# Optimization experiments

Hardware: AMD Instinct MI355X
Metric: run time of the kernel (lower is better)

Reference implementation:

```python
import jax, jax.numpy as jnp
import numpy as np

MAX_LENGTH = 10
SOS = 0


def setup_inputs() -> dict:
    key = jax.random.key(0)
    ks = jax.random.split(key, 16)
    B, S, H, V = 64, 128, 1024, 32000
    sc = 0.02
    return {
        "encoder_outputs": jax.random.normal(ks[0], (B, S, H), jnp.float32),
        "encoder_hidden": jax.random.normal(ks[1], (1, B, H), jnp.float32),
        "target_tensor": jax.random.randint(ks[2], (B, MAX_LENGTH), 0, V),
        "embedding": jax.random.normal(ks[3], (V, H), jnp.float32) * sc,
        "Wa_w": jax.random.normal(ks[4], (H, H), jnp.float32) * sc,
        "Wa_b": jnp.zeros((H,), jnp.float32),
        "Ua_w": jax.random.normal(ks[5], (H, H), jnp.float32) * sc,
        "Ua_b": jnp.zeros((H,), jnp.float32),
        "Va_w": jax.random.normal(ks[6], (1, H), jnp.float32) * sc,
        "Va_b": jnp.zeros((1,), jnp.float32),
        "gru_wi": jax.random.normal(ks[7], (3 * H, 2 * H), jnp.float32) * sc,
        "gru_wh": jax.random.normal(ks[8], (3 * H, H), jnp.float32) * sc,
        "gru_bi": jnp.zeros((3 * H,), jnp.float32),
        "gru_bh": jnp.zeros((3 * H,), jnp.float32),
        "out_w": jax.random.normal(ks[9], (V, H), jnp.float32) * sc,
        "out_b": jnp.zeros((V,), jnp.float32),
    }


def reference(encoder_outputs, encoder_hidden, target_tensor, embedding,
              Wa_w, Wa_b, Ua_w, Ua_b, Va_w, Va_b,
              gru_wi, gru_wh, gru_bi, gru_bh, out_w, out_b):
    B, S, H = encoder_outputs.shape
    # teacher-forced input tokens: [SOS, tgt_0, ..., tgt_{T-2}]
    tokens = jnp.concatenate(
        [jnp.full((B, 1), SOS, dtype=target_tensor.dtype),
         target_tensor[:, :MAX_LENGTH - 1]], axis=1)  # [B, T]
    emb_seq = embedding[tokens]                         # [B, T, H] (dropout = identity)
    # precompute Ua(keys), shared across steps
    Ua_keys = jnp.einsum('bsh,kh->bsk', encoder_outputs, Ua_w) + Ua_b  # [B,S,H]
    va = Va_w[0]

    def step(h, emb_t):  # h: [B,H], emb_t: [B,H]
        q = h @ Wa_w.T + Wa_b                                   # [B,H]
        scores = jnp.einsum('bsh,h->bs', jnp.tanh(q[:, None, :] + Ua_keys), va) + Va_b[0]
        w = jax.nn.softmax(scores, axis=-1)                     # [B,S]
        ctx = jnp.einsum('bs,bsh->bh', w, encoder_outputs)      # [B,H]
        x = jnp.concatenate([emb_t, ctx], axis=-1)              # [B,2H]
        gi = x @ gru_wi.T + gru_bi                              # [B,3H]
        gh = h @ gru_wh.T + gru_bh
        r = jax.nn.sigmoid(gi[:, :H] + gh[:, :H])
        z = jax.nn.sigmoid(gi[:, H:2 * H] + gh[:, H:2 * H])
        n = jnp.tanh(gi[:, 2 * H:] + r * gh[:, 2 * H:])
        h_new = (1.0 - z) * n + z * h
        return h_new, (h_new, w)

    h0 = encoder_hidden[0]  # [B,H]
    h_final, (outs, attns) = jax.lax.scan(step, h0, jnp.swapaxes(emb_seq, 0, 1))
    outs = jnp.swapaxes(outs, 0, 1)                 # [B,T,H]
    attns = jnp.swapaxes(attns, 0, 1)               # [B,T,S]
    logits = jnp.einsum('bth,vh->btv', outs, out_w) + out_b
    log_probs = jax.nn.log_softmax(logits, axis=-1)  # [B,T,V]
    return log_probs, h_final[None], attns
```

## Files before the change

kernel.cpp:

```cpp
#include <hip/hip_runtime.h>
#include <hip/hip_bf16.h>
#include <cstddef>

#define B 64
#define S 128
#define H 1024
#define V 32000
#define T 10
#define H3 3072
#define NCHUNK 250

typedef __bf16 bf16x8 __attribute__((ext_vector_type(8)));
typedef float f32x4 __attribute__((ext_vector_type(4)));
typedef unsigned short ushort8v __attribute__((ext_vector_type(8)));

__device__ inline unsigned short f2b(float f) {
    __hip_bfloat16 h = __float2bfloat16(f);
    return *reinterpret_cast<unsigned short*>(&h);
}
__device__ inline float b2f(unsigned short u) {
    return __uint_as_float(((unsigned)u) << 16);
}
__device__ inline float fast_tanh(float x) {
    float e = __expf(2.f * x);
    return 1.f - 2.f * __builtin_amdgcn_rcpf(e + 1.f);
}
__device__ inline float fast_sigmoid(float x) {
    return __builtin_amdgcn_rcpf(1.f + __expf(-x));
}

__device__ inline int xcd_swz(int orig, int nwg) {
    int q = nwg >> 3, r = nwg & 7;
    int xcd = orig & 7, idx = orig >> 3;
    int base = (xcd < r) ? xcd * (q + 1) : r * (q + 1) + (xcd - r) * q;
    return base + idx;
}

#define PREP_NB 52240
__global__ void prep_kernel(const float* __restrict__ enc, unsigned short* __restrict__ enc_bf,
                            const float* __restrict__ out_w, unsigned short* __restrict__ outw_bf,
                            const float* __restrict__ Ua_w, unsigned short* __restrict__ Ua_bf,
                            const float* __restrict__ gwh, const float* __restrict__ Wa_w,
                            unsigned short* __restrict__ Wcat,
                            const float* __restrict__ gwi,
                            unsigned short* __restrict__ Wemb, unsigned short* __restrict__ Wctx,
                            const float* __restrict__ gbh, const float* __restrict__ Wa_b,
                            float* __restrict__ catbias,
                            const float* __restrict__ emb, const int* __restrict__ tgt,
                            unsigned short* __restrict__ embg,
                            const float* __restrict__ h0, unsigned short* __restrict__ hbf,
                            float* __restrict__ hbuf) {
    const int bid = blockIdx.x, tid = threadIdx.x;
    if (bid < 8192) {
        int i = bid * 256 + tid;
        float4 v = reinterpret_cast<const float4*>(enc)[i];
        ushort4 o = { f2b(v.x), f2b(v.y), f2b(v.z), f2b(v.w) };
        reinterpret_cast<ushort4*>(enc_bf)[i] = o;
    } else if (bid < 40192) {
        int i = (bid - 8192) * 256 + tid;
        float4 v = reinterpret_cast<const float4*>(out_w)[i];
        ushort4 o = { f2b(v.x), f2b(v.y), f2b(v.z), f2b(v.w) };
        reinterpret_cast<ushort4*>(outw_bf)[i] = o;
    } else if (bid < 41216) {
        int i = (bid - 40192) * 256 + tid;
        float4 v = reinterpret_cast<const float4*>(Ua_w)[i];
        ushort4 o = { f2b(v.x), f2b(v.y), f2b(v.z), f2b(v.w) };
        reinterpret_cast<ushort4*>(Ua_bf)[i] = o;
    } else if (bid < 45312) {
        int i = (bid - 41216) * 256 + tid;
        int e = i * 4, n = e >> 10, k = e & 1023;
        const float* src = (n < H3) ? (gwh + (size_t)n * H + k) : (Wa_w + (size_t)(n - H3) * H + k);
        float4 v = *reinterpret_cast<const float4*>(src);
        ushort4 o = { f2b(v.x), f2b(v.y), f2b(v.z), f2b(v.w) };
        reinterpret_cast<ushort4*>(Wcat)[i] = o;
    } else if (bid < 48384) {
        int i = (bid - 45312) * 256 + tid;
        int e = i * 4, n = e >> 10, k = e & 1023;
        float4 v = *reinterpret_cast<const float4*>(gwi + (size_t)n * 2 * H + k);
        ushort4 o = { f2b(v.x), f2b(v.y), f2b(v.z), f2b(v.w) };
        reinterpret_cast<ushort4*>(Wemb)[i] = o;
    } else if (bid < 51456) {
        int i = (bid - 48384) * 256 + tid;
        int e = i * 4, n = e >> 10, k = e & 1023;
        float4 v = *reinterpret_cast<const float4*>(gwi + (size_t)n * 2 * H + H + k);
        ushort4 o = { f2b(v.x), f2b(v.y), f2b(v.z), f2b(v.w) };
        reinterpret_cast<ushort4*>(Wctx)[i] = o;
    } else if (bid < 51472) {
        int n = (bid - 51456) * 256 + tid;
        catbias[n] = (n < H3) ? gbh[n] : Wa_b[n - H3];
    } else if (bid < 52112) {
        int i = (bid - 51472) * 256 + tid;
        int e = i * 4;
        int t = e >> 16, rem = e & 65535;
        int b = rem >> 10, j = rem & 1023;
        int tok = (t == 0) ? 0 : tgt[b * T + (t - 1)];
        float4 v = *reinterpret_cast<const float4*>(emb + (size_t)tok * H + j);
        ushort4 o = { f2b(v.x), f2b(v.y), f2b(v.z), f2b(v.w) };
        *reinterpret_cast<ushort4*>(embg + ((size_t)t * B + b) * H + j) = o;
    } else if (bid < 52176) {
        int i = (bid - 52112) * 256 + tid;
        float4 v = reinterpret_cast<const float4*>(h0)[i];
        ushort4 o = { f2b(v.x), f2b(v.y), f2b(v.z), f2b(v.w) };
        reinterpret_cast<ushort4*>(hbf)[i] = o;
    } else {
        int i = (bid - 52176) * 256 + tid;
        reinterpret_cast<float4*>(hbuf)[i] = reinterpret_cast<const float4*>(h0)[i];
    }
}

struct GemmDesc {
    const unsigned short* A;
    const unsigned short* Bw;
    const float* bias;
    void* C;
    int M, N, out_bf16;
};

__global__ __launch_bounds__(512) void gemm3_kernel(GemmDesc d0, GemmDesc d1, GemmDesc d2) {
    __shared__ unsigned short As[128][72];
    __shared__ unsigned short Bs[128][72];
    const int bid = blockIdx.x;
    GemmDesc d; int local, nwg;
    if (bid < 512)       { d = d0; local = bid;        nwg = 512;  }
    else if (bid < 2048) { d = d1; local = bid - 512;  nwg = 1536; }
    else                 { d = d2; local = bid - 2048; nwg = 120;  }
    local = xcd_swz(local, nwg);
    const int mtiles = d.M >> 7;
    const int bm = (local % mtiles) << 7, bn = (local / mtiles) << 7;
    const int tid = threadIdx.x, lane = tid & 63, w = tid >> 6;
    const int wm = w >> 2, wn = w & 3;
    const int quad = lane >> 4, fr = lane & 15;
    f32x4 acc[4][2] = {};

    const int srow = tid >> 2, sc16 = (tid & 3) * 16;
    for (int k0 = 0; k0 < H; k0 += 64) {
        const unsigned short* ap = d.A + (size_t)(bm + srow) * H + k0 + sc16;
        *reinterpret_cast<bf16x8*>(&As[srow][sc16])     = *reinterpret_cast<const bf16x8*>(ap);
        *reinterpret_cast<bf16x8*>(&As[srow][sc16 + 8]) = *reinterpret_cast<const bf16x8*>(ap + 8);
        const unsigned short* bp = d.Bw + (size_t)(bn + srow) * H + k0 + sc16;
        *reinterpret_cast<bf16x8*>(&Bs[srow][sc16])     = *reinterpret_cast<const bf16x8*>(bp);
        *reinterpret_cast<bf16x8*>(&Bs[srow][sc16 + 8]) = *reinterpret_cast<const bf16x8*>(bp + 8);
        __syncthreads();
        #pragma unroll
        for (int ks = 0; ks < 2; ++ks) {
            const int kg = quad * 8 + 32 * ks;
            bf16x8 a[4], bb[2];
            #pragma unroll
            for (int m = 0; m < 4; ++m)
                a[m] = *reinterpret_cast<const bf16x8*>(&As[64 * wm + 16 * m + fr][kg]);
            #pragma unroll
            for (int n = 0; n < 2; ++n)
                bb[n] = *reinterpret_cast<const bf16x8*>(&Bs[32 * wn + 16 * n + fr][kg]);
            #pragma unroll
            for (int m = 0; m < 4; ++m)
                #pragma unroll
                for (int n = 0; n < 2; ++n)
                    acc[m][n] = __builtin_amdgcn_mfma_f32_16x16x32_bf16(a[m], bb[n], acc[m][n], 0, 0, 0);
        }
        __syncthreads();
    }
    #pragma unroll
    for (int n = 0; n < 2; ++n) {
        int col = bn + 32 * wn + 16 * n + fr;
        float bv = d.bias ? d.bias[col] : 0.f;
        #pragma unroll
        for (int m = 0; m < 4; ++m)
            #pragma unroll
            for (int i = 0; i < 4; ++i) {
                int row = bm + 64 * wm + 16 * m + quad * 4 + i;
                float v = acc[m][n][i] + bv;
                if (d.out_bf16)
                    ((unsigned short*)d.C)[(size_t)row * d.N + col] = f2b(v);
                else
                    ((float*)d.C)[(size_t)row * d.N + col] = v;
            }
    }
}

__global__ __launch_bounds__(512) void gemm_logits(const unsigned short* __restrict__ A,
                                                   const unsigned short* __restrict__ Bw,
                                                   const float* __restrict__ bias,
                                                   float* __restrict__ Cout,
                                                   float2* __restrict__ stats,
                                                   int M, int N, int K) {
    __shared__ unsigned short As[128][72];
    __shared__ unsigned short Bs[128][72];
    __shared__ float mred[128][4];
    __shared__ float sred[128][4];
    const int wg = xcd_swz(blockIdx.x, gridDim.x);
    const int mtiles = M >> 7;
    const int bm = (wg % mtiles) << 7, bn = (wg / mtiles) << 7;
    const int tid = threadIdx.x, lane = tid & 63, w = tid >> 6;
    const int wm = w >> 2, wn = w & 3;
    const int quad = lane >> 4, fr = lane & 15;
    f32x4 acc[4][2] = {};

    const int srow = tid >> 2, sc16 = (tid & 3) * 16;
    for (int k0 = 0; k0 < K; k0 += 64) {
        const unsigned short* ap = A + (size_t)(bm + srow) * K + k0 + sc16;
        *reinterpret_cast<bf16x8*>(&As[srow][sc16])     = *reinterpret_cast<const bf16x8*>(ap);
        *reinterpret_cast<bf16x8*>(&As[srow][sc16 + 8]) = *reinterpret_cast<const bf16x8*>(ap + 8);
        const unsigned short* bp = Bw + (size_t)(bn + srow) * K + k0 + sc16;
        *reinterpret_cast<bf16x8*>(&Bs[srow][sc16])     = *reinterpret_cast<const bf16x8*>(bp);
        *reinterpret_cast<bf16x8*>(&Bs[srow][sc16 + 8]) = *reinterpret_cast<const bf16x8*>(bp + 8);
        __syncthreads();
        #pragma unroll
        for (int ks = 0; ks < 2; ++ks) {
            const int kg = quad * 8 + 32 * ks;
            bf16x8 a[4], bb[2];
            #pragma unroll
            for (int m = 0; m < 4; ++m)
                a[m] = *reinterpret_cast<const bf16x8*>(&As[64 * wm + 16 * m + fr][kg]);
            #pragma unroll
            for (int n = 0; n < 2; ++n)
                bb[n] = *reinterpret_cast<const bf16x8*>(&Bs[32 * wn + 16 * n + fr][kg]);
            #pragma unroll
            for (int m = 0; m < 4; ++m)
                #pragma unroll
                for (int n = 0; n < 2; ++n)
                    acc[m][n] = __builtin_amdgcn_mfma_f32_16x16x32_bf16(a[m], bb[n], acc[m][n], 0, 0, 0);
        }
        __syncthreads();
    }

    #pragma unroll
    for (int n = 0; n < 2; ++n) {
        int col = bn + 32 * wn + 16 * n + fr;
        float bv = bias[col];
        #pragma unroll
        for (int m = 0; m < 4; ++m)
            #pragma unroll
            for (int i = 0; i < 4; ++i) {
                int row = bm + 64 * wm + 16 * m + quad * 4 + i;
                float v = acc[m][n][i] + bv;
                Cout[(size_t)row * N + col] = v;
                acc[m][n][i] = v;
            }
    }

    const int nchunk = N >> 7;
    #pragma unroll
    for (int m = 0; m < 4; ++m)
        #pragma unroll
        for (int i = 0; i < 4; ++i) {
            float x = fmaxf(acc[m][0][i], acc[m][1][i]);
            x = fmaxf(x, __shfl_xor(x, 1)); x = fmaxf(x, __shfl_xor(x, 2));
            x = fmaxf(x, __shfl_xor(x, 4)); x = fmaxf(x, __shfl_xor(x, 8));
            if (fr == 0) mred[64 * wm + 16 * m + quad * 4 + i][wn] = x;
        }
    __syncthreads();
    #pragma unroll
    for (int m = 0; m < 4; ++m)
        #pragma unroll
        for (int i = 0; i < 4; ++i) {
            int rl = 64 * wm + 16 * m + quad * 4 + i;
            float Mr = fmaxf(fmaxf(mred[rl][0], mred[rl][1]), fmaxf(mred[rl][2], mred[rl][3]));
            float sv = expf(acc[m][0][i] - Mr) + expf(acc[m][1][i] - Mr);
            sv += __shfl_xor(sv, 1); sv += __shfl_xor(sv, 2);
            sv += __shfl_xor(sv, 4); sv += __shfl_xor(sv, 8);
            if (fr == 0) sred[rl][wn] = sv;
        }
    __syncthreads();
    if (tid < 128) {
        float Mr = fmaxf(fmaxf(mred[tid][0], mred[tid][1]), fmaxf(mred[tid][2], mred[tid][3]));
        float Sv = sred[tid][0] + sred[tid][1] + sred[tid][2] + sred[tid][3];
        stats[(size_t)(bm + tid) * nchunk + (bn >> 7)] = make_float2(Mr, Sv);
    }
}

__global__ __launch_bounds__(256) void gemm_smallA(const unsigned short* __restrict__ A,
                                                   const unsigned short* __restrict__ Bw,
                                                   const float* __restrict__ bias,
                                                   float* __restrict__ Cout) {
    __shared__ unsigned short As[64][136];
    __shared__ unsigned short Bs[32][136];
    const int bn = blockIdx.x * 32;
    const int tid = threadIdx.x, lane = tid & 63, w = tid >> 6;
    const int quad = lane >> 4, fr = lane & 15;
    f32x4 acc[2] = {};

    const int srA = tid >> 2, scA = (tid & 3) * 32;
    const int srB = tid >> 3, scB = (tid & 7) * 16;
    for (int k0 = 0; k0 < H; k0 += 128) {
        const unsigned short* ap = A + (size_t)srA * H + k0 + scA;
        #pragma unroll
        for (int u = 0; u < 4; ++u)
            *reinterpret_cast<bf16x8*>(&As[srA][scA + 8 * u]) =
                *reinterpret_cast<const bf16x8*>(ap + 8 * u);
        const unsigned short* bp = Bw + (size_t)(bn + srB) * H + k0 + scB;
        *reinterpret_cast<bf16x8*>(&Bs[srB][scB])     = *reinterpret_cast<const bf16x8*>(bp);
        *reinterpret_cast<bf16x8*>(&Bs[srB][scB + 8]) = *reinterpret_cast<const bf16x8*>(bp + 8);
        __syncthreads();
        #pragma unroll
        for (int ks = 0; ks < 4; ++ks) {
            const int kg = quad * 8 + 32 * ks;
            bf16x8 a = *reinterpret_cast<const bf16x8*>(&As[16 * w + fr][kg]);
            #pragma unroll
            for (int n = 0; n < 2; ++n) {
                bf16x8 bb = *reinterpret_cast<const bf16x8*>(&Bs[16 * n + fr][kg]);
                acc[n] = __builtin_amdgcn_mfma_f32_16x16x32_bf16(a, bb, acc[n], 0, 0, 0);
            }
        }
        __syncthreads();
    }
    #pragma unroll
    for (int n = 0; n < 2; ++n) {
        int col = bn + 16 * n + fr;
        float bv = bias[col];
        #pragma unroll
        for (int i = 0; i < 4; ++i) {
            int row = 16 * w + quad * 4 + i;
            Cout[(size_t)row * 4096 + col] = acc[n][i] + bv;
        }
    }
}

__global__ __launch_bounds__(256) void stepB(const float* __restrict__ ghq,
                                             const unsigned short* __restrict__ keys,
                                             const unsigned short* __restrict__ KV,
                                             const float* __restrict__ va,
                                             const float* __restrict__ va_b,
                                             const float* __restrict__ gi_emb,
                                             float* __restrict__ h,
                                             unsigned short* __restrict__ hbf,
                                             unsigned short* __restrict__ outs_bf,
                                             float* __restrict__ attns,
                                             float* __restrict__ h_final, int t) {
    const int q = blockIdx.x, b = blockIdx.y;
    const int tid = threadIdx.x, lane = tid & 63, wv = tid >> 6;
    __shared__ float ssc[128];
    __shared__ float sw[128];
    __shared__ float red[4][64][13];

    float qv[16], vv[16];
    {
        const float* qp = ghq + (size_t)b * 4096 + H3 + lane * 16;
        const float* vp = va + lane * 16;
        #pragma unroll
        for (int j = 0; j < 16; ++j) { qv[j] = qp[j]; vv[j] = vp[j]; }
    }
    const float vab = va_b[0];
    const unsigned short* kb = keys + (size_t)b * S * H;
    for (int i = 0; i < 32; i += 2) {
        int s0 = wv * 32 + i;
        const unsigned short* kr0 = kb + (size_t)s0 * H + lane * 16;
        const unsigned short* kr1 = kr0 + H;
        ushort8v k00 = *reinterpret_cast<const ushort8v*>(kr0);
        ushort8v k01 = *reinterpret_cast<const ushort8v*>(kr0 + 8);
        ushort8v k10 = *reinterpret_cast<const ushort8v*>(kr1);
        ushort8v k11 = *reinterpret_cast<const ushort8v*>(kr1 + 8);
        float a0 = 0.f, a1 = 0.f;
        #pragma unroll
        for (int e = 0; e < 8; ++e) {
            a0 += fast_tanh(qv[e] + b2f(k00[e])) * vv[e];
            a1 += fast_tanh(qv[e] + b2f(k10[e])) * vv[e];
        }
        #pragma unroll
        for (int e = 0; e < 8; ++e) {
            a0 += fast_tanh(qv[8 + e] + b2f(k01[e])) * vv[8 + e];
            a1 += fast_tanh(qv[8 + e] + b2f(k11[e])) * vv[8 + e];
        }
        a0 += __shfl_xor(a0, 1);  a1 += __shfl_xor(a1, 1);
        a0 += __shfl_xor(a0, 2);  a1 += __shfl_xor(a1, 2);
        a0 += __shfl_xor(a0, 4);  a1 += __shfl_xor(a1, 4);
        a0 += __shfl_xor(a0, 8);  a1 += __shfl_xor(a1, 8);
        a0 += __shfl_xor(a0, 16); a1 += __shfl_xor(a1, 16);
        a0 += __shfl_xor(a0, 32); a1 += __shfl_xor(a1, 32);
        if (lane == 0) { ssc[s0] = a0 + vab; ssc[s0 + 1] = a1 + vab; }
    }
    __syncthreads();
    if (tid < 128) {
        float mx = -1e30f;
        #pragma unroll 8
        for (int s = 0; s < 128; ++s) mx = fmaxf(mx, ssc[s]);
        float sum = 0.f;
        #pragma unroll 8
        for (int s = 0; s < 128; ++s) sum += __expf(ssc[s] - mx);
        float wvv = __expf(ssc[tid] - mx) / sum;
        sw[tid] = wvv;
        if (q == 0) attns[((size_t)b * T + t) * S + tid] = wvv;
    }
    __syncthreads();

    const int j0 = q * 256 + lane * 4;
    float ar[4] = {}, az[4] = {}, an[4] = {};
    const unsigned short* kvb = KV + (size_t)b * S * H3 + j0;
    for (int i = 0; i < 32; i += 2) {
        int s0 = wv * 32 + i;
        float w0 = sw[s0], w1 = sw[s0 + 1];
        const unsigned short* r0 = kvb + (size_t)s0 * H3;
        const unsigned short* r1 = r0 + H3;
        uint2 u0a = *reinterpret_cast<const uint2*>(r0);
        uint2 u1a = *reinterpret_cast<const uint2*>(r0 + 1024);
        uint2 u2a = *reinterpret_cast<const uint2*>(r0 + 2048);
        uint2 u0b = *reinterpret_cast<const uint2*>(r1);
        uint2 u1b = *reinterpret_cast<const uint2*>(r1 + 1024);
        uint2 u2b = *reinterpret_cast<const uint2*>(r1 + 2048);
        ar[0] += w0 * b2f((unsigned short)(u0a.x & 0xffff)) + w1 * b2f((unsigned short)(u0b.x & 0xffff));
        ar[1] += w0 * b2f((unsigned short)(u0a.x >> 16))    + w1 * b2f((unsigned short)(u0b.x >> 16));
        ar[2] += w0 * b2f((unsigned short)(u0a.y & 0xffff)) + w1 * b2f((unsigned short)(u0b.y & 0xffff));
        ar[3] += w0 * b2f((unsigned short)(u0a.y >> 16))    + w1 * b2f((unsigned short)(u0b.y >> 16));
        az[0] += w0 * b2f((unsigned short)(u1a.x & 0xffff)) + w1 * b2f((unsigned short)(u1b.x & 0xffff));
        az[1] += w0 * b2f((unsigned short)(u1a.x >> 16))    + w1 * b2f((unsigned short)(u1b.x >> 16));
        az[2] += w0 * b2f((unsigned short)(u1a.y & 0xffff)) + w1 * b2f((unsigned short)(u1b.y & 0xffff));
        az[3] += w0 * b2f((unsigned short)(u1a.y >> 16))    + w1 * b2f((unsigned short)(u1b.y >> 16));
        an[0] += w0 * b2f((unsigned short)(u2a.x & 0xffff)) + w1 * b2f((unsigned short)(u2b.x & 0xffff));
        an[1] += w0 * b2f((unsigned short)(u2a.x >> 16))    + w1 * b2f((unsigned short)(u2b.x >> 16));
        an[2] += w0 * b2f((unsigned short)(u2a.y & 0xffff)) + w1 * b2f((unsigned short)(u2b.y & 0xffff));
        an[3] += w0 * b2f((unsigned short)(u2a.y >> 16))    + w1 * b2f((unsigned short)(u2b.y >> 16));
    }
    #pragma unroll
    for (int g = 0; g < 4; ++g) {
        red[wv][lane][g]     = ar[g];
        red[wv][lane][4 + g] = az[g];
        red[wv][lane][8 + g] = an[g];
    }
    __syncthreads();

    if (tid < 64) {
        float rr[4], zz[4], nn[4];
        #pragma unroll
        for (int g = 0; g < 4; ++g) {
            rr[g] = red[0][tid][g] + red[1][tid][g] + red[2][tid][g] + red[3][tid][g];
            zz[g] = red[0][tid][4+g] + red[1][tid][4+g] + red[2][tid][4+g] + red[3][tid][4+g];
            nn[g] = red[0][tid][8+g] + red[1][tid][8+g] + red[2][tid][8+g] + red[3][tid][8+g];
        }
        const int jj = q * 256 + tid * 4;
        const float* ge = gi_emb + ((size_t)t * B + b) * H3;
        const float* gh = ghq + (size_t)b * 4096;
        float geR[4], geZ[4], geN[4], ghR[4], ghZ[4], ghN[4], hv[4];
        *reinterpret_cast<float4*>(geR) = *reinterpret_cast<const float4*>(ge + jj);
        *reinterpret_cast<float4*>(geZ) = *reinterpret_cast<const float4*>(ge + 1024 + jj);
        *reinterpret_cast<float4*>(geN) = *reinterpret_cast<const float4*>(ge + 2048 + jj);
        *reinterpret_cast<float4*>(ghR) = *reinterpret_cast<const float4*>(gh + jj);
        *reinterpret_cast<float4*>(ghZ) = *reinterpret_cast<const float4*>(gh + 1024 + jj);
        *reinterpret_cast<float4*>(ghN) = *reinterpret_cast<const float4*>(gh + 2048 + jj);
        *reinterpret_cast<float4*>(hv)  = *reinterpret_cast<const float4*>(h + (size_t)b * H + jj);
        ushort4 hb;
        unsigned short* hbp = reinterpret_cast<unsigned short*>(&hb);
        #pragma unroll
        for (int i = 0; i < 4; ++i) {
            float r = fast_sigmoid(geR[i] + rr[i] + ghR[i]);
            float z = fast_sigmoid(geZ[i] + zz[i] + ghZ[i]);
            float n = fast_tanh(geN[i] + nn[i] + r * ghN[i]);
            hv[i] = (1.f - z) * n + z * hv[i];
            hbp[i] = f2b(hv[i]);
        }
        *reinterpret_cast<float4*>(h + (size_t)b * H + jj) = *reinterpret_cast<float4*>(hv);
        *reinterpret_cast<ushort4*>(hbf + (size_t)b * H + jj) = hb;
        *reinterpret_cast<ushort4*>(outs_bf + ((size_t)b * T + t) * H + jj) = hb;
        if (t == T - 1)
            *reinterpret_cast<float4*>(h_final + (size_t)b * H + jj) = *reinterpret_cast<float4*>(hv);
    }
}

__global__ void lsesub_kernel(const float2* __restrict__ stats, float* __restrict__ x) {
    const int row = blockIdx.x;
    const int tid = threadIdx.x;
    __shared__ float shm[256];
    __shared__ float shs[256];
    float mv = -1e30f, sv = 0.f;
    float2 st = make_float2(-1e30f, 0.f);
    if (tid < NCHUNK) { st = stats[(size_t)row * NCHUNK + tid]; mv = st.x; }
    shm[tid] = mv; __syncthreads();
    for (int off = 128; off > 0; off >>= 1) {
        if (tid < off) shm[tid] = fmaxf(shm[tid], shm[tid + off]);
        __syncthreads();
    }
    float M = shm[0]; __syncthreads();
    if (tid < NCHUNK) sv = st.y * expf(st.x - M);
    shs[tid] = sv; __syncthreads();
    for (int off = 128; off > 0; off >>= 1) {
        if (tid < off) shs[tid] += shs[tid + off];
        __syncthreads();
    }
    float L = M + logf(shs[0]);
    __syncthreads();
    float4* p = reinterpret_cast<float4*>(x + (size_t)row * V);
    for (int i = tid; i < V / 4; i += 256) {
        float4 v = p[i];
        v.x -= L; v.y -= L; v.z -= L; v.w -= L;
        p[i] = v;
    }
}


extern "C" void kernel_launch(void* const* d_in, const int* in_sizes, int n_in,
                              void* d_out, int out_size, void* d_ws, size_t ws_size,
                              hipStream_t stream) {
    const float* enc   = (const float*)d_in[0];
    const float* h0    = (const float*)d_in[1];
    const int*   tgt   = (const int*)d_in[2];
    const float* emb   = (const float*)d_in[3];
    const float* Wa_w  = (const float*)d_in[4];
    const float* Wa_b  = (const float*)d_in[5];
    const float* Ua_w  = (const float*)d_in[6];
    const float* Ua_b  = (const float*)d_in[7];
    const float* Va_w  = (const float*)d_in[8];
    const float* Va_b  = (const float*)d_in[9];
    const float* gwi   = (const float*)d_in[10];
    const float* gwh   = (const float*)d_in[11];
    const float* gbi   = (const float*)d_in[12];
    const float* gbh   = (const float*)d_in[13];
    const float* out_w = (const float*)d_in[14];
    const float* out_b = (const float*)d_in[15];

    float* out       = (float*)d_out;
    float* log_probs = out;
    float* h_final   = out + (size_t)B * T * V;
    float* attns     = h_final + (size_t)B * H;

    char* pp = (char*)d_ws;
    auto alloc = [&](size_t bytes) { char* r = pp; pp += (bytes + 255) & ~(size_t)255; return r; };
    unsigned short* ua_bf   = (unsigned short*)alloc((size_t)B * S * H * 2);
    unsigned short* enc_bf  = (unsigned short*)alloc((size_t)B * S * H * 2);
    unsigned short* outw_bf = (unsigned short*)alloc((size_t)V * H * 2);
    unsigned short* KV      = (unsigned short*)alloc((size_t)B * S * H3 * 2);
    unsigned short* Ua_bf   = (unsigned short*)alloc((size_t)H * H * 2);
    unsigned short* Wcat    = (unsigned short*)alloc((size_t)4096 * H * 2);
    unsigned short* Wctx    = (unsigned short*)alloc((size_t)H3 * H * 2);
    unsigned short* Wemb    = (unsigned short*)alloc((size_t)H3 * H * 2);
    float*          catbias = (float*)alloc(4096 * 4);
    unsigned short* embg    = (unsigned short*)alloc((size_t)T * B * H * 2);
    float*          gi_emb  = (float*)alloc((size_t)T * B * H3 * 4);
    float*          hbuf    = (float*)alloc((size_t)B * H * 4);
    unsigned short* hbf     = (unsigned short*)alloc((size_t)B * H * 2);
    float*          ghq     = (float*)alloc((size_t)B * 4096 * 4);
    unsigned short* outs_bf = (unsigned short*)alloc((size_t)B * T * H * 2);
    float2*         stats   = (float2*)alloc((size_t)B * T * NCHUNK * 8);

    prep_kernel<<<PREP_NB, 256, 0, stream>>>(enc, enc_bf, out_w, outw_bf, Ua_w, Ua_bf,
                                             gwh, Wa_w, Wcat, gwi, Wemb, Wctx,
                                             gbh, Wa_b, catbias, emb, tgt, embg,
                                             h0, hbf, hbuf);

    GemmDesc d0 = { enc_bf, Ua_bf, Ua_b, (void*)ua_bf,  B * S, H,  1 };
    GemmDesc d1 = { enc_bf, Wctx,  nullptr, (void*)KV,  B * S, H3, 1 };
    GemmDesc d2 = { embg,   Wemb,  gbi, (void*)gi_emb,  T * B, H3, 0 };
    gemm3_kernel<<<2168, 512, 0, stream>>>(d0, d1, d2);

    for (int t = 0; t < T; ++t) {
        gemm_smallA<<<128, 256, 0, stream>>>(hbf, Wcat, catbias, ghq);
        stepB<<<dim3(4, B), 256, 0, stream>>>(ghq, ua_bf, KV, Va_w, Va_b, gi_emb,
                                              hbuf, hbf, outs_bf, attns, h_final, t);
    }

    gemm_logits<<<(B * T / 128) * (V / 128), 512, 0, stream>>>(
        outs_bf, outw_bf, out_b, log_probs, stats, B * T, V, H);
    lsesub_kernel<<<B * T, 256, 0, stream>>>(stats, log_probs);
}
```

Baseline: 711.6 us.

## Fuse per-step GEMM and attention/GRU via grid barrier; overlap out_w conversion with GEMMs

The two per-timestep kernels (a small h×[Wgh;Wa] GEMM and the attention+GRU update) are merged into a single 256-block kernel. The blocks synchronize through an atomic-counter grid barrier, with a separate counter per step, and exchange ghq through system-scope atomic loads and stores. This halves the launches in the recurrent loop and removes the inter-kernel gaps. Separately, the bf16 conversion of out_w moves out of the prep kernel into extra blocks of the batched GEMM launch, so it can overlap with GEMM work. The spin barrier relies on all 256 blocks being co-resident, and the scalarized atomic loads may be slower than vector loads.

```diff
diff --git a/kernel.cpp b/kernel.cpp
--- a/kernel.cpp
+++ b/kernel.cpp
@@ -9,6 +9,7 @@
 #define T 10
 #define H3 3072
 #define NCHUNK 250
+#define SK_NB 256
 
 typedef __bf16 bf16x8 __attribute__((ext_vector_type(8)));
 typedef float f32x4 __attribute__((ext_vector_type(4)));
@@ -27,6 +28,18 @@
 }
 __device__ inline float fast_sigmoid(float x) {
     return __builtin_amdgcn_rcpf(1.f + __expf(-x));
+}
+__device__ inline float2 sysload_f2(const float* p) {
+    unsigned long long v = __hip_atomic_load((const unsigned long long*)p,
+                                             __ATOMIC_RELAXED, __HIP_MEMORY_SCOPE_SYSTEM);
+    float2 r;
+    r.x = __uint_as_float((unsigned)v);
+    r.y = __uint_as_float((unsigned)(v >> 32));
+    return r;
+}
+__device__ inline void sysstore_f(float* p, float v) {
+    __hip_atomic_store((unsigned*)p, __float_as_uint(v),
+                       __ATOMIC_RELAXED, __HIP_MEMORY_SCOPE_SYSTEM);
 }
 
 __device__ inline int xcd_swz(int orig, int nwg) {
@@ -36,9 +49,8 @@
     return base + idx;
 }
 
-#define PREP_NB 52240
+#define PREP_NB 20240
 __global__ void prep_kernel(const float* __restrict__ enc, unsigned short* __restrict__ enc_bf,
-                            const float* __restrict__ out_w, unsigned short* __restrict__ outw_bf,
                             const float* __restrict__ Ua_w, unsigned short* __restrict__ Ua_bf,
                             const float* __restrict__ gwh, const float* __restrict__ Wa_w,
                             unsigned short* __restrict__ Wcat,
@@ -56,40 +68,35 @@
         float4 v = reinterpret_cast<const float4*>(enc)[i];
         ushort4 o = { f2b(v.x), f2b(v.y), f2b(v.z), f2b(v.w) };
         reinterpret_cast<ushort4*>(enc_bf)[i] = o;
-    } else if (bid < 40192) {
+    } else if (bid < 9216) {
         int i = (bid - 8192) * 256 + tid;
-        float4 v = reinterpret_cast<const float4*>(out_w)[i];
-        ushort4 o = { f2b(v.x), f2b(v.y), f2b(v.z), f2b(v.w) };
-        reinterpret_cast<ushort4*>(outw_bf)[i] = o;
-    } else if (bid < 41216) {
-        int i = (bid - 40192) * 256 + tid;
         float4 v = reinterpret_cast<const float4*>(Ua_w)[i];
         ushort4 o = { f2b(v.x), f2b(v.y), f2b(v.z), f2b(v.w) };
         reinterpret_cast<ushort4*>(Ua_bf)[i] = o;
-    } else if (bid < 45312) {
-        int i = (bid - 41216) * 256 + tid;
+    } else if (bid < 13312) {
+        int i = (bid - 9216) * 256 + tid;
         int e = i * 4, n = e >> 10, k = e & 1023;
         const float* src = (n < H3) ? (gwh + (size_t)n * H + k) : (Wa_w + (size_t)(n - H3) * H + k);
         float4 v = *reinterpret_cast<const float4*>(src);
         ushort4 o = { f2b(v.x), f2b(v.y), f2b(v.z), f2b(v.w) };
         reinterpret_cast<ushort4*>(Wcat)[i] = o;
-    } else if (bid < 48384) {
-        int i = (bid - 45312) * 256 + tid;
+    } else if (bid < 16384) {
+        int i = (bid - 13312) * 256 + tid;
         int e = i * 4, n = e >> 10, k = e & 1023;
         float4 v = *reinterpret_cast<const float4*>(gwi + (size_t)n * 2 * H + k);
         ushort4 o = { f2b(v.x), f2b(v.y), f2b(v.z), f2b(v.w) };
         reinterpret_cast<ushort4*>(Wemb)[i] = o;
-    } else if (bid < 51456) {
-        int i = (bid - 48384) * 256 + tid;
+    } else if (bid < 19456) {
+        int i = (bid - 16384) * 256 + tid;
         int e = i * 4, n = e >> 10, k = e & 1023;
         float4 v = *reinterpret_cast<const float4*>(gwi + (size_t)n * 2 * H + H + k);
         ushort4 o = { f2b(v.x), f2b(v.y), f2b(v.z), f2b(v.w) };
         reinterpret_cast<ushort4*>(Wctx)[i] = o;
-    } else if (bid < 51472) {
-        int n = (bid - 51456) * 256 + tid;
+    } else if (bid < 19472) {
+        int n = (bid - 19456) * 256 + tid;
         catbias[n] = (n < H3) ? gbh[n] : Wa_b[n - H3];
-    } else if (bid < 52112) {
-        int i = (bid - 51472) * 256 + tid;
+    } else if (bid < 20112) {
+        int i = (bid - 19472) * 256 + tid;
         int e = i * 4;
         int t = e >> 16, rem = e & 65535;
         int b = rem >> 10, j = rem & 1023;
@@ -97,13 +104,13 @@
         float4 v = *reinterpret_cast<const float4*>(emb + (size_t)tok * H + j);
         ushort4 o = { f2b(v.x), f2b(v.y), f2b(v.z), f2b(v.w) };
         *reinterpret_cast<ushort4*>(embg + ((size_t)t * B + b) * H + j) = o;
-    } else if (bid < 52176) {
-        int i = (bid - 52112) * 256 + tid;
+    } else if (bid < 20176) {
+        int i = (bid - 20112) * 256 + tid;
         float4 v = reinterpret_cast<const float4*>(h0)[i];
         ushort4 o = { f2b(v.x), f2b(v.y), f2b(v.z), f2b(v.w) };
         reinterpret_cast<ushort4*>(hbf)[i] = o;
     } else {
-        int i = (bid - 52176) * 256 + tid;
+        int i = (bid - 20176) * 256 + tid;
         reinterpret_cast<float4*>(hbuf)[i] = reinterpret_cast<const float4*>(h0)[i];
     }
 }
@@ -116,10 +123,20 @@
     int M, N, out_bf16;
 };
 
-__global__ __launch_bounds__(512) void gemm3_kernel(GemmDesc d0, GemmDesc d1, GemmDesc d2) {
+__global__ __launch_bounds__(512) void gemm3_kernel(GemmDesc d0, GemmDesc d1, GemmDesc d2,
+                                                    const float* __restrict__ out_w,
+                                                    unsigned short* __restrict__ outw_bf) {
     __shared__ unsigned short As[128][72];
     __shared__ unsigned short Bs[128][72];
     const int bid = blockIdx.x;
+    const int tid = threadIdx.x;
+    if (bid >= 2168) {
+        int i = (bid - 2168) * 512 + tid;
+        float4 v = reinterpret_cast<const float4*>(out_w)[i];
+        ushort4 o = { f2b(v.x), f2b(v.y), f2b(v.z), f2b(v.w) };
+        reinterpret_cast<ushort4*>(outw_bf)[i] = o;
+        return;
+    }
     GemmDesc d; int local, nwg;
     if (bid < 512)       { d = d0; local = bid;        nwg = 512;  }
     else if (bid < 2048) { d = d1; local = bid - 512;  nwg = 1536; }
@@ -127,7 +144,7 @@
     local = xcd_swz(local, nwg);
     const int mtiles = d.M >> 7;
     const int bm = (local % mtiles) << 7, bn = (local / mtiles) << 7;
-    const int tid = threadIdx.x, lane = tid & 63, w = tid >> 6;
+    const int lane = tid & 63, w = tid >> 6;
     const int wm = w >> 2, wn = w & 3;
     const int quad = lane >> 4, fr = lane & 15;
     f32x4 acc[4][2] = {};
@@ -268,76 +285,83 @@
     }
 }
 
-__global__ __launch_bounds__(256) void gemm_smallA(const unsigned short* __restrict__ A,
-                                                   const unsigned short* __restrict__ Bw,
-                                                   const float* __restrict__ bias,
-                                                   float* __restrict__ Cout) {
+__global__ __launch_bounds__(256) void step_kernel(const unsigned short* __restrict__ hbf_in,
+                                                   const unsigned short* __restrict__ Wcat,
+                                                   const float* __restrict__ catbias,
+                                                   float* __restrict__ ghq,
+                                                   const unsigned short* __restrict__ keys,
+                                                   const unsigned short* __restrict__ KV,
+                                                   const float* __restrict__ va,
+                                                   const float* __restrict__ va_b,
+                                                   const float* __restrict__ gi_emb,
+                                                   float* __restrict__ h,
+                                                   unsigned short* __restrict__ hbf_out,
+                                                   unsigned short* __restrict__ outs_bf,
+                                                   float* __restrict__ attns,
+                                                   float* __restrict__ h_final,
+                                                   unsigned int* __restrict__ ctr, int t) {
     __shared__ unsigned short As[64][136];
-    __shared__ unsigned short Bs[32][136];
-    const int bn = blockIdx.x * 32;
-    const int tid = threadIdx.x, lane = tid & 63, w = tid >> 6;
-    const int quad = lane >> 4, fr = lane & 15;
-    f32x4 acc[2] = {};
-
-    const int srA = tid >> 2, scA = (tid & 3) * 32;
-    const int srB = tid >> 3, scB = (tid & 7) * 16;
-    for (int k0 = 0; k0 < H; k0 += 128) {
-        const unsigned short* ap = A + (size_t)srA * H + k0 + scA;
-        #pragma unroll
-        for (int u = 0; u < 4; ++u)
-            *reinterpret_cast<bf16x8*>(&As[srA][scA + 8 * u]) =
-                *reinterpret_cast<const bf16x8*>(ap + 8 * u);
-        const unsigned short* bp = Bw + (size_t)(bn + srB) * H + k0 + scB;
-        *reinterpret_cast<bf16x8*>(&Bs[srB][scB])     = *reinterpret_cast<const bf16x8*>(bp);
-        *reinterpret_cast<bf16x8*>(&Bs[srB][scB + 8]) = *reinterpret_cast<const bf16x8*>(bp + 8);
-        __syncthreads();
-        #pragma unroll
-        for (int ks = 0; ks < 4; ++ks) {
-            const int kg = quad * 8 + 32 * ks;
-            bf16x8 a = *reinterpret_cast<const bf16x8*>(&As[16 * w + fr][kg]);
-            #pragma unroll
-            for (int n = 0; n < 2; ++n) {
-                bf16x8 bb = *reinterpret_cast<const bf16x8*>(&Bs[16 * n + fr][kg]);
-                acc[n] = __builtin_amdgcn_mfma_f32_16x16x32_bf16(a, bb, acc[n], 0, 0, 0);
-            }
-        }
-        __syncthreads();
-    }
-    #pragma unroll
-    for (int n = 0; n < 2; ++n) {
-        int col = bn + 16 * n + fr;
-        float bv = bias[col];
-        #pragma unroll
-        for (int i = 0; i < 4; ++i) {
-            int row = 16 * w + quad * 4 + i;
-            Cout[(size_t)row * 4096 + col] = acc[n][i] + bv;
-        }
-    }
-}
-
-__global__ __launch_bounds__(256) void stepB(const float* __restrict__ ghq,
-                                             const unsigned short* __restrict__ keys,
-                                             const unsigned short* __restrict__ KV,
-                                             const float* __restrict__ va,
-                                             const float* __restrict__ va_b,
-                                             const float* __restrict__ gi_emb,
-                                             float* __restrict__ h,
-                                             unsigned short* __restrict__ hbf,
-                                             unsigned short* __restrict__ outs_bf,
-                                             float* __restrict__ attns,
-                                             float* __restrict__ h_final, int t) {
-    const int q = blockIdx.x, b = blockIdx.y;
-    const int tid = threadIdx.x, lane = tid & 63, wv = tid >> 6;
+    __shared__ unsigned short Bsm[16][136];
     __shared__ float ssc[128];
     __shared__ float sw[128];
     __shared__ float red[4][64][13];
-
+    const int bid = blockIdx.x;
+    const int tid = threadIdx.x, lane = tid & 63, wv = tid >> 6;
+    const int quad = lane >> 4, fr = lane & 15;
+
+    {
+        const int bn = bid * 16;
+        f32x4 acc = {};
+        const int srA = tid >> 2, scA = (tid & 3) * 32;
+        const int srB = tid >> 4, scB = (tid & 15) * 8;
+        for (int k0 = 0; k0 < H; k0 += 128) {
+            const unsigned short* ap = hbf_in + (size_t)srA * H + k0 + scA;
+            #pragma unroll
+            for (int u = 0; u < 4; ++u)
+                *reinterpret_cast<bf16x8*>(&As[srA][scA + 8 * u]) =
+                    *reinterpret_cast<const bf16x8*>(ap + 8 * u);
+            const unsigned short* bp = Wcat + (size_t)(bn + srB) * H + k0 + scB;
+            *reinterpret_cast<bf16x8*>(&Bsm[srB][scB]) = *reinterpret_cast<const bf16x8*>(bp);
+            __syncthreads();
+            #pragma unroll
+            for (int ks = 0; ks < 4; ++ks) {
+                const int kg = quad * 8 + 32 * ks;
+                bf16x8 a = *reinterpret_cast<const bf16x8*>(&As[16 * wv + fr][kg]);
+                bf16x8 bb = *reinterpret_cast<const bf16x8*>(&Bsm[fr][kg]);
+                acc = __builtin_amdgcn_mfma_f32_16x16x32_bf16(a, bb, acc, 0, 0, 0);
+            }
+            __syncthreads();
+        }
+        int col = bn + fr;
+        float bv = catbias[col];
+        #pragma unroll
+        for (int i = 0; i < 4; ++i) {
+            int row = 16 * wv + quad * 4 + i;
+            sysstore_f(&ghq[(size_t)row * 4096 + col], acc[i] + bv);
+        }
+    }
+
+    __syncthreads();
+    if (tid == 0) {
+        atomicAdd(ctr, 1u);
+        while (__hip_atomic_load(ctr, __ATOMIC_RELAXED, __HIP_MEMORY_SCOPE_AGENT) < SK_NB)
+            __builtin_amdgcn_s_sleep(1);
+    }
+    __syncthreads();
+    asm volatile("" ::: "memory");
+
+    const int q = bid & 3, b = bid >> 2;
     float qv[16], vv[16];
     {
         const float* qp = ghq + (size_t)b * 4096 + H3 + lane * 16;
         const float* vp = va + lane * 16;
         #pragma unroll
-        for (int j = 0; j < 16; ++j) { qv[j] = qp[j]; vv[j] = vp[j]; }
+        for (int j = 0; j < 8; ++j) {
+            float2 f = sysload_f2(qp + j * 2);
+            qv[j * 2] = f.x; qv[j * 2 + 1] = f.y;
+        }
+        #pragma unroll
+        for (int j = 0; j < 16; ++j) vv[j] = vp[j];
     }
     const float vab = va_b[0];
     const unsigned short* kb = keys + (size_t)b * S * H;
@@ -432,10 +456,14 @@
         *reinterpret_cast<float4*>(geR) = *reinterpret_cast<const float4*>(ge + jj);
         *reinterpret_cast<float4*>(geZ) = *reinterpret_cast<const float4*>(ge + 1024 + jj);
         *reinterpret_cast<float4*>(geN) = *reinterpret_cast<const float4*>(ge + 2048 + jj);
-        *reinterpret_cast<float4*>(ghR) = *reinterpret_cast<const float4*>(gh + jj);
-        *reinterpret_cast<float4*>(ghZ) = *reinterpret_cast<const float4*>(gh + 1024 + jj);
-        *reinterpret_cast<float4*>(ghN) = *reinterpret_cast<const float4*>(gh + 2048 + jj);
-        *reinterpret_cast<float4*>(hv)  = *reinterpret_cast<const float4*>(h + (size_t)b * H + jj);
+        float2 f;
+        f = sysload_f2(gh + jj);            ghR[0] = f.x; ghR[1] = f.y;
+        f = sysload_f2(gh + jj + 2);        ghR[2] = f.x; ghR[3] = f.y;
+        f = sysload_f2(gh + 1024 + jj);     ghZ[0] = f.x; ghZ[1] = f.y;
+        f = sysload_f2(gh + 1024 + jj + 2); ghZ[2] = f.x; ghZ[3] = f.y;
+        f = sysload_f2(gh + 2048 + jj);     ghN[0] = f.x; ghN[1] = f.y;
+        f = sysload_f2(gh + 2048 + jj + 2); ghN[2] = f.x; ghN[3] = f.y;
+        *reinterpret_cast<float4*>(hv) = *reinterpret_cast<const float4*>(h + (size_t)b * H + jj);
         ushort4 hb;
         unsigned short* hbp = reinterpret_cast<unsigned short*>(&hb);
         #pragma unroll
@@ -447,7 +475,7 @@
             hbp[i] = f2b(hv[i]);
         }
         *reinterpret_cast<float4*>(h + (size_t)b * H + jj) = *reinterpret_cast<float4*>(hv);
-        *reinterpret_cast<ushort4*>(hbf + (size_t)b * H + jj) = hb;
+        *reinterpret_cast<ushort4*>(hbf_out + (size_t)b * H + jj) = hb;
         *reinterpret_cast<ushort4*>(outs_bf + ((size_t)b * T + t) * H + jj) = hb;
         if (t == T - 1)
             *reinterpret_cast<float4*>(h_final + (size_t)b * H + jj) = *reinterpret_cast<float4*>(hv);
@@ -528,8 +556,11 @@
     float*          ghq     = (float*)alloc((size_t)B * 4096 * 4);
     unsigned short* outs_bf = (unsigned short*)alloc((size_t)B * T * H * 2);
     float2*         stats   = (float2*)alloc((size_t)B * T * NCHUNK * 8);
-
-    prep_kernel<<<PREP_NB, 256, 0, stream>>>(enc, enc_bf, out_w, outw_bf, Ua_w, Ua_bf,
+    unsigned int*   ctrs    = (unsigned int*)alloc(T * 4);
+
+    hipMemsetAsync(ctrs, 0, T * sizeof(unsigned int), stream);
+
+    prep_kernel<<<PREP_NB, 256, 0, stream>>>(enc, enc_bf, Ua_w, Ua_bf,
                                              gwh, Wa_w, Wcat, gwi, Wemb, Wctx,
                                              gbh, Wa_b, catbias, emb, tgt, embg,
                                              h0, hbf, hbuf);
@@ -537,12 +568,12 @@
     GemmDesc d0 = { enc_bf, Ua_bf, Ua_b, (void*)ua_bf,  B * S, H,  1 };
     GemmDesc d1 = { enc_bf, Wctx,  nullptr, (void*)KV,  B * S, H3, 1 };
     GemmDesc d2 = { embg,   Wemb,  gbi, (void*)gi_emb,  T * B, H3, 0 };
-    gemm3_kernel<<<2168, 512, 0, stream>>>(d0, d1, d2);
+    gemm3_kernel<<<18168, 512, 0, stream>>>(d0, d1, d2, out_w, outw_bf);
 
     for (int t = 0; t < T; ++t) {
-        gemm_smallA<<<128, 256, 0, stream>>>(hbf, Wcat, catbias, ghq);
-        stepB<<<dim3(4, B), 256, 0, stream>>>(ghq, ua_bf, KV, Va_w, Va_b, gi_emb,
-                                              hbuf, hbf, outs_bf, attns, h_final, t);
+        step_kernel<<<SK_NB, 256, 0, stream>>>(hbf, Wcat, catbias, ghq, ua_bf, KV,
+                                               Va_w, Va_b, gi_emb, hbuf, hbf, outs_bf,
+                                               attns, h_final, ctrs + t, t);
     }
 
     gemm_logits<<<(B * T / 128) * (V / 128), 512, 0, stream>>>(
```

New measurement: 734.7 us. +3.3%, slower.

## Stage GEMM tiles via direct global-to-LDS loads and overlap out_w conversion

Applied to the files above, without the earlier changes.

The bf16 GEMM kernels now load A/B tiles with global_load_lds straight into unpadded 32-wide LDS tiles, replacing register-staged 64-wide copies into padded tiles. The out_w fp32-to-bf16 conversion moves out of prep_kernel and becomes extra tail blocks of gemm3_kernel, so it can run alongside the attention-precompute GEMMs. The aim is to cut VGPR staging cost and shrink the serial prep phase. In exchange the K loop has twice as many barriers per tile, and the unpadded LDS layout may cause bank conflicts on fragment reads.

```diff
diff --git a/kernel.cpp b/kernel.cpp
--- a/kernel.cpp
+++ b/kernel.cpp
@@ -29,6 +29,12 @@
     return __builtin_amdgcn_rcpf(1.f + __expf(-x));
 }
 
+__device__ inline void gload_lds16(const void* g, void* l) {
+    __builtin_amdgcn_global_load_lds(
+        (const __attribute__((address_space(1))) void*)g,
+        (__attribute__((address_space(3))) void*)l, 16, 0, 0);
+}
+
 __device__ inline int xcd_swz(int orig, int nwg) {
     int q = nwg >> 3, r = nwg & 7;
     int xcd = orig & 7, idx = orig >> 3;
@@ -36,9 +42,8 @@
     return base + idx;
 }
 
-#define PREP_NB 52240
+#define PREP_NB 20240
 __global__ void prep_kernel(const float* __restrict__ enc, unsigned short* __restrict__ enc_bf,
-                            const float* __restrict__ out_w, unsigned short* __restrict__ outw_bf,
                             const float* __restrict__ Ua_w, unsigned short* __restrict__ Ua_bf,
                             const float* __restrict__ gwh, const float* __restrict__ Wa_w,
                             unsigned short* __restrict__ Wcat,
@@ -56,40 +61,35 @@
         float4 v = reinterpret_cast<const float4*>(enc)[i];
         ushort4 o = { f2b(v.x), f2b(v.y), f2b(v.z), f2b(v.w) };
         reinterpret_cast<ushort4*>(enc_bf)[i] = o;
-    } else if (bid < 40192) {
+    } else if (bid < 9216) {
         int i = (bid - 8192) * 256 + tid;
-        float4 v = reinterpret_cast<const float4*>(out_w)[i];
-        ushort4 o = { f2b(v.x), f2b(v.y), f2b(v.z), f2b(v.w) };
-        reinterpret_cast<ushort4*>(outw_bf)[i] = o;
-    } else if (bid < 41216) {
-        int i = (bid - 40192) * 256 + tid;
         float4 v = reinterpret_cast<const float4*>(Ua_w)[i];
         ushort4 o = { f2b(v.x), f2b(v.y), f2b(v.z), f2b(v.w) };
         reinterpret_cast<ushort4*>(Ua_bf)[i] = o;
-    } else if (bid < 45312) {
-        int i = (bid - 41216) * 256 + tid;
+    } else if (bid < 13312) {
+        int i = (bid - 9216) * 256 + tid;
         int e = i * 4, n = e >> 10, k = e & 1023;
         const float* src = (n < H3) ? (gwh + (size_t)n * H + k) : (Wa_w + (size_t)(n - H3) * H + k);
         float4 v = *reinterpret_cast<const float4*>(src);
         ushort4 o = { f2b(v.x), f2b(v.y), f2b(v.z), f2b(v.w) };
         reinterpret_cast<ushort4*>(Wcat)[i] = o;
-    } else if (bid < 48384) {
-        int i = (bid - 45312) * 256 + tid;
+    } else if (bid < 16384) {
+        int i = (bid - 13312) * 256 + tid;
         int e = i * 4, n = e >> 10, k = e & 1023;
         float4 v = *reinterpret_cast<const float4*>(gwi + (size_t)n * 2 * H + k);
         ushort4 o = { f2b(v.x), f2b(v.y), f2b(v.z), f2b(v.w) };
         reinterpret_cast<ushort4*>(Wemb)[i] = o;
-    } else if (bid < 51456) {
-        int i = (bid - 48384) * 256 + tid;
+    } else if (bid < 19456) {
+        int i = (bid - 16384) * 256 + tid;
         int e = i * 4, n = e >> 10, k = e & 1023;
         float4 v = *reinterpret_cast<const float4*>(gwi + (size_t)n * 2 * H + H + k);
         ushort4 o = { f2b(v.x), f2b(v.y), f2b(v.z), f2b(v.w) };
         reinterpret_cast<ushort4*>(Wctx)[i] = o;
-    } else if (bid < 51472) {
-        int n = (bid - 51456) * 256 + tid;
+    } else if (bid < 19472) {
+        int n = (bid - 19456) * 256 + tid;
         catbias[n] = (n < H3) ? gbh[n] : Wa_b[n - H3];
-    } else if (bid < 52112) {
-        int i = (bid - 51472) * 256 + tid;
+    } else if (bid < 20112) {
+        int i = (bid - 19472) * 256 + tid;
         int e = i * 4;
         int t = e >> 16, rem = e & 65535;
         int b = rem >> 10, j = rem & 1023;
@@ -97,13 +97,13 @@
         float4 v = *reinterpret_cast<const float4*>(emb + (size_t)tok * H + j);
         ushort4 o = { f2b(v.x), f2b(v.y), f2b(v.z), f2b(v.w) };
         *reinterpret_cast<ushort4*>(embg + ((size_t)t * B + b) * H + j) = o;
-    } else if (bid < 52176) {
-        int i = (bid - 52112) * 256 + tid;
+    } else if (bid < 20176) {
+        int i = (bid - 20112) * 256 + tid;
         float4 v = reinterpret_cast<const float4*>(h0)[i];
         ushort4 o = { f2b(v.x), f2b(v.y), f2b(v.z), f2b(v.w) };
         reinterpret_cast<ushort4*>(hbf)[i] = o;
     } else {
-        int i = (bid - 52176) * 256 + tid;
+        int i = (bid - 20176) * 256 + tid;
         reinterpret_cast<float4*>(hbuf)[i] = reinterpret_cast<const float4*>(h0)[i];
     }
 }
@@ -116,10 +116,20 @@
     int M, N, out_bf16;
 };
 
-__global__ __launch_bounds__(512) void gemm3_kernel(GemmDesc d0, GemmDesc d1, GemmDesc d2) {
-    __shared__ unsigned short As[128][72];
-    __shared__ unsigned short Bs[128][72];
+__global__ __launch_bounds__(512) void gemm3_kernel(GemmDesc d0, GemmDesc d1, GemmDesc d2,
+                                                    const float* __restrict__ out_w,
+                                                    unsigned short* __restrict__ outw_bf) {
+    __shared__ unsigned short As[128 * 32];
+    __shared__ unsigned short Bs[128 * 32];
     const int bid = blockIdx.x;
+    const int tid = threadIdx.x;
+    if (bid >= 2168) {
+        int i = (bid - 2168) * 512 + tid;
+        float4 v = reinterpret_cast<const float4*>(out_w)[i];
+        ushort4 o = { f2b(v.x), f2b(v.y), f2b(v.z), f2b(v.w) };
+        reinterpret_cast<ushort4*>(outw_bf)[i] = o;
+        return;
+    }
     GemmDesc d; int local, nwg;
     if (bid < 512)       { d = d0; local = bid;        nwg = 512;  }
     else if (bid < 2048) { d = d1; local = bid - 512;  nwg = 1536; }
@@ -127,36 +137,35 @@
     local = xcd_swz(local, nwg);
     const int mtiles = d.M >> 7;
     const int bm = (local % mtiles) << 7, bn = (local / mtiles) << 7;
-    const int tid = threadIdx.x, lane = tid & 63, w = tid >> 6;
+    const int lane = tid & 63, w = tid >> 6;
     const int wm = w >> 2, wn = w & 3;
     const int quad = lane >> 4, fr = lane & 15;
+    const int K = H;
     f32x4 acc[4][2] = {};
 
-    const int srow = tid >> 2, sc16 = (tid & 3) * 16;
-    for (int k0 = 0; k0 < H; k0 += 64) {
-        const unsigned short* ap = d.A + (size_t)(bm + srow) * H + k0 + sc16;
-        *reinterpret_cast<bf16x8*>(&As[srow][sc16])     = *reinterpret_cast<const bf16x8*>(ap);
-        *reinterpret_cast<bf16x8*>(&As[srow][sc16 + 8]) = *reinterpret_cast<const bf16x8*>(ap + 8);
-        const unsigned short* bp = d.Bw + (size_t)(bn + srow) * H + k0 + sc16;
-        *reinterpret_cast<bf16x8*>(&Bs[srow][sc16])     = *reinterpret_cast<const bf16x8*>(bp);
-        *reinterpret_cast<bf16x8*>(&Bs[srow][sc16 + 8]) = *reinterpret_cast<const bf16x8*>(bp + 8);
-        __syncthreads();
-        #pragma unroll
-        for (int ks = 0; ks < 2; ++ks) {
-            const int kg = quad * 8 + 32 * ks;
-            bf16x8 a[4], bb[2];
-            #pragma unroll
-            for (int m = 0; m < 4; ++m)
-                a[m] = *reinterpret_cast<const bf16x8*>(&As[64 * wm + 16 * m + fr][kg]);
+    const int sr = w * 16 + (lane >> 2), sc = (lane & 3) * 8;
+    const unsigned short* agp = d.A + (size_t)(bm + sr) * K + sc;
+    const unsigned short* bgp = d.Bw + (size_t)(bn + sr) * K + sc;
+    unsigned short* alp = As + w * 512;
+    unsigned short* blp = Bs + w * 512;
+
+    for (int k0 = 0; k0 < K; k0 += 32) {
+        gload_lds16(agp + k0, alp);
+        gload_lds16(bgp + k0, blp);
+        __syncthreads();
+        const int kg = quad * 8;
+        bf16x8 a[4], bb[2];
+        #pragma unroll
+        for (int m = 0; m < 4; ++m)
+            a[m] = *reinterpret_cast<const bf16x8*>(&As[(64 * wm + 16 * m + fr) * 32 + kg]);
+        #pragma unroll
+        for (int n = 0; n < 2; ++n)
+            bb[n] = *reinterpret_cast<const bf16x8*>(&Bs[(32 * wn + 16 * n + fr) * 32 + kg]);
+        #pragma unroll
+        for (int m = 0; m < 4; ++m)
             #pragma unroll
             for (int n = 0; n < 2; ++n)
-                bb[n] = *reinterpret_cast<const bf16x8*>(&Bs[32 * wn + 16 * n + fr][kg]);
-            #pragma unroll
-            for (int m = 0; m < 4; ++m)
-                #pragma unroll
-                for (int n = 0; n < 2; ++n)
-                    acc[m][n] = __builtin_amdgcn_mfma_f32_16x16x32_bf16(a[m], bb[n], acc[m][n], 0, 0, 0);
-        }
+                acc[m][n] = __builtin_amdgcn_mfma_f32_16x16x32_bf16(a[m], bb[n], acc[m][n], 0, 0, 0);
         __syncthreads();
     }
     #pragma unroll
@@ -183,8 +192,8 @@
                                                    float* __restrict__ Cout,
                                                    float2* __restrict__ stats,
                                                    int M, int N, int K) {
-    __shared__ unsigned short As[128][72];
-    __shared__ unsigned short Bs[128][72];
+    __shared__ unsigned short As[128 * 32];
+    __shared__ unsigned short Bs[128 * 32];
     __shared__ float mred[128][4];
     __shared__ float sred[128][4];
     const int wg = xcd_swz(blockIdx.x, gridDim.x);
@@ -195,31 +204,29 @@
     const int quad = lane >> 4, fr = lane & 15;
     f32x4 acc[4][2] = {};
 
-    const int srow = tid >> 2, sc16 = (tid & 3) * 16;
-    for (int k0 = 0; k0 < K; k0 += 64) {
-        const unsigned short* ap = A + (size_t)(bm + srow) * K + k0 + sc16;
-        *reinterpret_cast<bf16x8*>(&As[srow][sc16])     = *reinterpret_cast<const bf16x8*>(ap);
-        *reinterpret_cast<bf16x8*>(&As[srow][sc16 + 8]) = *reinterpret_cast<const bf16x8*>(ap + 8);
-        const unsigned short* bp = Bw + (size_t)(bn + srow) * K + k0 + sc16;
-        *reinterpret_cast<bf16x8*>(&Bs[srow][sc16])     = *reinterpret_cast<const bf16x8*>(bp);
-        *reinterpret_cast<bf16x8*>(&Bs[srow][sc16 + 8]) = *reinterpret_cast<const bf16x8*>(bp + 8);
-        __syncthreads();
-        #pragma unroll
-        for (int ks = 0; ks < 2; ++ks) {
-            const int kg = quad * 8 + 32 * ks;
-            bf16x8 a[4], bb[2];
-            #pragma unroll
-            for (int m = 0; m < 4; ++m)
-                a[m] = *reinterpret_cast<const bf16x8*>(&As[64 * wm + 16 * m + fr][kg]);
+    const int sr = w * 16 + (lane >> 2), sc = (lane & 3) * 8;
+    const unsigned short* agp = A + (size_t)(bm + sr) * K + sc;
+    const unsigned short* bgp = Bw + (size_t)(bn + sr) * K + sc;
+    unsigned short* alp = As + w * 512;
+    unsigned short* blp = Bs + w * 512;
+
+    for (int k0 = 0; k0 < K; k0 += 32) {
+        gload_lds16(agp + k0, alp);
+        gload_lds16(bgp + k0, blp);
+        __syncthreads();
+        const int kg = quad * 8;
+        bf16x8 a[4], bb[2];
+        #pragma unroll
+        for (int m = 0; m < 4; ++m)
+            a[m] = *reinterpret_cast<const bf16x8*>(&As[(64 * wm + 16 * m + fr) * 32 + kg]);
+        #pragma unroll
+        for (int n = 0; n < 2; ++n)
+            bb[n] = *reinterpret_cast<const bf16x8*>(&Bs[(32 * wn + 16 * n + fr) * 32 + kg]);
+        #pragma unroll
+        for (int m = 0; m < 4; ++m)
             #pragma unroll
             for (int n = 0; n < 2; ++n)
-                bb[n] = *reinterpret_cast<const bf16x8*>(&Bs[32 * wn + 16 * n + fr][kg]);
-            #pragma unroll
-            for (int m = 0; m < 4; ++m)
-                #pragma unroll
-                for (int n = 0; n < 2; ++n)
-                    acc[m][n] = __builtin_amdgcn_mfma_f32_16x16x32_bf16(a[m], bb[n], acc[m][n], 0, 0, 0);
-        }
+                acc[m][n] = __builtin_amdgcn_mfma_f32_16x16x32_bf16(a[m], bb[n], acc[m][n], 0, 0, 0);
         __syncthreads();
     }
 
@@ -529,7 +536,7 @@
     unsigned short* outs_bf = (unsigned short*)alloc((size_t)B * T * H * 2);
     float2*         stats   = (float2*)alloc((size_t)B * T * NCHUNK * 8);
 
-    prep_kernel<<<PREP_NB, 256, 0, stream>>>(enc, enc_bf, out_w, outw_bf, Ua_w, Ua_bf,
+    prep_kernel<<<PREP_NB, 256, 0, stream>>>(enc, enc_bf, Ua_w, Ua_bf,
                                              gwh, Wa_w, Wcat, gwi, Wemb, Wctx,
                                              gbh, Wa_b, catbias, emb, tgt, embg,
                                              h0, hbf, hbuf);
@@ -537,7 +544,7 @@
     GemmDesc d0 = { enc_bf, Ua_bf, Ua_b, (void*)ua_bf,  B * S, H,  1 };
     GemmDesc d1 = { enc_bf, Wctx,  nullptr, (void*)KV,  B * S, H3, 1 };
     GemmDesc d2 = { embg,   Wemb,  gbi, (void*)gi_emb,  T * B, H3, 0 };
-    gemm3_kernel<<<2168, 512, 0, stream>>>(d0, d1, d2);
+    gemm3_kernel<<<18168, 512, 0, stream>>>(d0, d1, d2, out_w, outw_bf);
 
     for (int t = 0; t < T; ++t) {
         gemm_smallA<<<128, 256, 0, stream>>>(hbf, Wcat, catbias, ghq);
```

Measured after the change: 712.3 us. Within noise of the previous version (+0.1%).
